# Kernel optimization log

Measured on AMD Instinct MI355X. Metric: run time of the kernel, lower is better.

The kernel has to match this reference:

```python
import jax, jax.numpy as jnp
import numpy as np

B, T1, T2, D = 16, 64, 64, 1024
PROJ = D // 2


def setup_inputs() -> dict:
    key = jax.random.key(0)
    k1, k2, k3 = jax.random.split(key, 3)
    x = jax.random.normal(k1, (B, T1, T2, D), dtype=jnp.float32)
    # glorot-style scale for params
    W_proj = jax.random.normal(k2, (D, PROJ), dtype=jnp.float32) * (2.0 / (D + PROJ)) ** 0.5
    v_score = jax.random.normal(k3, (PROJ,), dtype=jnp.float32) * (1.0 / PROJ) ** 0.5
    return {"x": x, "W_proj": W_proj, "v_score": v_score}


def reference(x, W_proj, v_score):
    # proj_input = tanh(tensordot(x, W_proj, axes=(3,0)))  -> (B, T1, T2, PROJ)
    proj = jnp.tanh(jnp.einsum('btsd,dp->btsp', x, W_proj))
    # att_scores = tensordot(proj, v_score, axes=(3,0))    -> (B, T1, T2)
    scores = jnp.einsum('btsp,p->bts', proj, v_score)
    # softmax over last axis (T2), weighted sum of x over T2 -> (B, T1, D)
    attn = jax.nn.softmax(scores, axis=-1)
    out = jnp.einsum('bts,btsd->btd', attn, x)
    return out
```

## Files before the change

### kernel.cpp

```cpp
#include <hip/hip_runtime.h>
#include <hip/hip_bf16.h>
#include <math.h>

#define B_    16
#define T1_   64
#define T2_   64
#define D_    1024
#define PROJ_ 512
#define BM    64
#define BK    32
#define NT    (D_ / BK)
#define LDP   40

typedef __attribute__((ext_vector_type(8))) short bf16x8;
typedef __attribute__((ext_vector_type(4))) float f32x4;
typedef __attribute__((ext_vector_type(4))) unsigned int u32x4;

__device__ __forceinline__ unsigned short f2bf(float f) {
  unsigned int u = __builtin_bit_cast(unsigned int, f);
  u += 0x7FFFu + ((u >> 16) & 1u);
  return (unsigned short)(u >> 16);
}

__device__ __forceinline__ float fast_tanh(float a) {
  float t = __builtin_amdgcn_exp2f(a * 2.885390081777927f);
  return 1.0f - 2.0f * __builtin_amdgcn_rcpf(t + 1.0f);
}

__global__ __launch_bounds__(256) void make_bfrag(
    const float* __restrict__ W, unsigned short* __restrict__ wt) {
  __shared__ float tile[32][33];
  const int t  = blockIdx.x;
  const int np = blockIdx.y;
  const int tx = threadIdx.x & 31;
  const int ty = threadIdx.x >> 5;
#pragma unroll
  for (int i = 0; i < 4; ++i)
    tile[ty + i * 8][tx] =
        W[(size_t)(t * 32 + ty + i * 8) * PROJ_ + np * 32 + tx];
  __syncthreads();
  if (threadIdx.x < 128) {
    const int sub  = threadIdx.x >> 6;
    const int lane = threadIdx.x & 63;
    const int llo = lane & 15, lhi = lane >> 4;
    unsigned short o[8];
#pragma unroll
    for (int j = 0; j < 8; ++j)
      o[j] = f2bf(tile[lhi * 8 + j][sub * 16 + llo]);
    const int n16 = np * 2 + sub;
    *(u32x4*)(wt + ((size_t)(t * 32 + n16) * 64 + lane) * 8) = *(const u32x4*)o;
  }
}

__global__ __launch_bounds__(512, 4) void fused_kernel(
    const float* __restrict__ x, const unsigned short* __restrict__ wt,
    const float* __restrict__ v, float* __restrict__ out) {
  __shared__ unsigned short As[2][BM][LDP];
  __shared__ float sp[BM][9];
  __shared__ float attn[BM];
  __shared__ f32x4 xred[256];

  const int tid  = threadIdx.x;
  const int lane = tid & 63;
  const int wid  = tid >> 6;
  const int llo  = lane & 15, lhi = lane >> 4;
  const int bt   = blockIdx.x;
  const int m0   = bt * BM;

  f32x4 acc[4][4];
#pragma unroll
  for (int mf = 0; mf < 4; ++mf)
#pragma unroll
    for (int nf = 0; nf < 4; ++nf) acc[mf][nf] = (f32x4){0.f, 0.f, 0.f, 0.f};

  const int arow = tid >> 3, akc = (tid & 7) * 4;
  const float* asrc = x + (size_t)(m0 + arow) * D_ + akc;

  const u32x4* wt4 = (const u32x4*)wt;
  const int bbase = (wid * 4) * 64 + lane;

  float4 s0 = *(const float4*)(asrc);
  float4 s1 = *(const float4*)(asrc + BK);
  u32x4 rb[4];
#pragma unroll
  for (int nf = 0; nf < 4; ++nf) rb[nf] = wt4[bbase + nf * 64];
  {
    ushort4 ua = {f2bf(s0.x), f2bf(s0.y), f2bf(s0.z), f2bf(s0.w)};
    *(ushort4*)&As[0][arow][akc] = ua;
  }

#define KSTEP(T, SLD, SCV, BR, BW)                                           \
  {                                                                          \
    __syncthreads();                                                         \
    bf16x8 af0 = *(const bf16x8*)&As[BR][ 0 + llo][lhi * 8];                 \
    bf16x8 af1 = *(const bf16x8*)&As[BR][16 + llo][lhi * 8];                 \
    bf16x8 af2 = *(const bf16x8*)&As[BR][32 + llo][lhi * 8];                 \
    bf16x8 af3 = *(const bf16x8*)&As[BR][48 + llo][lhi * 8];                 \
    if ((T) + 2 < NT) SLD = *(const float4*)(asrc + ((T) + 2) * BK);         \
    _Pragma("unroll")                                                        \
    for (int nf = 0; nf < 4; ++nf) {                                         \
      bf16x8 bfr = *(const bf16x8*)&rb[nf];                                  \
      acc[0][nf] = __builtin_amdgcn_mfma_f32_16x16x32_bf16(af0, bfr, acc[0][nf], 0, 0, 0); \
      acc[1][nf] = __builtin_amdgcn_mfma_f32_16x16x32_bf16(af1, bfr, acc[1][nf], 0, 0, 0); \
      acc[2][nf] = __builtin_amdgcn_mfma_f32_16x16x32_bf16(af2, bfr, acc[2][nf], 0, 0, 0); \
      acc[3][nf] = __builtin_amdgcn_mfma_f32_16x16x32_bf16(af3, bfr, acc[3][nf], 0, 0, 0); \
      if ((T) + 1 < NT) rb[nf] = wt4[bbase + ((T) + 1) * 2048 + nf * 64];    \
    }                                                                        \
    if ((T) + 1 < NT) {                                                      \
      ushort4 ua = {f2bf(SCV.x), f2bf(SCV.y), f2bf(SCV.z), f2bf(SCV.w)};     \
      *(ushort4*)&As[BW][arow][akc] = ua;                                    \
    }                                                                        \
  }

  for (int t = 0; t < NT; t += 2) {
    KSTEP(t,     s0, s1, 0, 1)
    KSTEP(t + 1, s1, s0, 1, 0)
  }
#undef KSTEP

  float vv0 = v[wid * 64 +  0 + llo];
  float vv1 = v[wid * 64 + 16 + llo];
  float vv2 = v[wid * 64 + 32 + llo];
  float vv3 = v[wid * 64 + 48 + llo];
#pragma unroll
  for (int mf = 0; mf < 4; ++mf) {
    float pr[4] = {0.f, 0.f, 0.f, 0.f};
#pragma unroll
    for (int r = 0; r < 4; ++r) {
      pr[r] += fast_tanh(acc[mf][0][r]) * vv0;
      pr[r] += fast_tanh(acc[mf][1][r]) * vv1;
      pr[r] += fast_tanh(acc[mf][2][r]) * vv2;
      pr[r] += fast_tanh(acc[mf][3][r]) * vv3;
    }
#pragma unroll
    for (int r = 0; r < 4; ++r) {
      float p = pr[r];
      p += __shfl_xor(p, 1, 64);
      p += __shfl_xor(p, 2, 64);
      p += __shfl_xor(p, 4, 64);
      p += __shfl_xor(p, 8, 64);
      if (llo == 0) sp[mf * 16 + lhi * 4 + r][wid] = p;
    }
  }
  __syncthreads();

  if (tid < BM) {
    float s = 0.f;
#pragma unroll
    for (int w = 0; w < 8; ++w) s += sp[tid][w];
    float mx = s;
#pragma unroll
    for (int mask = 1; mask < 64; mask <<= 1)
      mx = fmaxf(mx, __shfl_xor(mx, mask, 64));
    const float e = __builtin_amdgcn_exp2f((s - mx) * 1.442695040888963f);
    float sum = e;
#pragma unroll
    for (int mask = 1; mask < 64; mask <<= 1)
      sum += __shfl_xor(sum, mask, 64);
    attn[tid] = e * __builtin_amdgcn_rcpf(sum);
  }
  __syncthreads();

  const int c4 = tid & 255;
  const int sh = tid >> 8;
  const float* xg = x + ((size_t)m0 + sh * 32) * D_ + c4 * 4;
  f32x4 o0 = {0.f,0.f,0.f,0.f}, o1 = o0, o2 = o0, o3 = o0;
#pragma unroll
  for (int s = 0; s < 32; s += 4) {
    const float w0 = attn[sh * 32 + s + 0];
    const float w1 = attn[sh * 32 + s + 1];
    const float w2 = attn[sh * 32 + s + 2];
    const float w3 = attn[sh * 32 + s + 3];
    const float4 a0 = *(const float4*)(xg + (size_t)(s + 0) * D_);
    const float4 a1 = *(const float4*)(xg + (size_t)(s + 1) * D_);
    const float4 a2 = *(const float4*)(xg + (size_t)(s + 2) * D_);
    const float4 a3 = *(const float4*)(xg + (size_t)(s + 3) * D_);
    o0[0] += w0 * a0.x; o0[1] += w0 * a0.y; o0[2] += w0 * a0.z; o0[3] += w0 * a0.w;
    o1[0] += w1 * a1.x; o1[1] += w1 * a1.y; o1[2] += w1 * a1.z; o1[3] += w1 * a1.w;
    o2[0] += w2 * a2.x; o2[1] += w2 * a2.y; o2[2] += w2 * a2.z; o2[3] += w2 * a2.w;
    o3[0] += w3 * a3.x; o3[1] += w3 * a3.y; o3[2] += w3 * a3.z; o3[3] += w3 * a3.w;
  }
  f32x4 o;
#pragma unroll
  for (int j = 0; j < 4; ++j) o[j] = (o0[j] + o1[j]) + (o2[j] + o3[j]);
  if (sh == 1) xred[c4] = o;
  __syncthreads();
  if (sh == 0) {
    f32x4 o2b = xred[c4];
    float4 res = {o[0] + o2b[0], o[1] + o2b[1], o[2] + o2b[2], o[3] + o2b[3]};
    *(float4*)(out + (size_t)bt * D_ + c4 * 4) = res;
  }
}

extern "C" void kernel_launch(void* const* d_in, const int* in_sizes, int n_in,
                              void* d_out, int out_size, void* d_ws, size_t ws_size,
                              hipStream_t stream) {
  const float* x = (const float*)d_in[0];
  const float* W = (const float*)d_in[1];
  const float* v = (const float*)d_in[2];
  float* out = (float*)d_out;
  unsigned short* Wt = (unsigned short*)d_ws;

  make_bfrag<<<dim3(NT, PROJ_ / 32), 256, 0, stream>>>(W, Wt);
  fused_kernel<<<B_ * T1_, 512, 0, stream>>>(x, Wt, v, out);
}
```

Measured before the change: 113.9 us.

## Stage half of the K dimension into swizzled LDS in bulk instead of per-step double buffering

Replaces the per-32-K double-buffered A tile, which needed a barrier every step, with two bulk stages that each convert 512 columns of the 64-row x tile to bf16 into a 64KB XOR-swizzled LDS buffer. The MFMA loop then runs 16 steps per half with no barriers, prefetches the next W fragments, and raises wave priority around the MFMAs. This removes most of the barriers but loses overlap between global loads and compute inside each half, and the 64KB LDS allocation lowers occupancy below the launch-bounds target of 4 blocks.

Result: slower. 128.9 us (+13.2%).

```diff
diff --git a/kernel.cpp b/kernel.cpp
--- a/kernel.cpp
+++ b/kernel.cpp
@@ -8,9 +8,8 @@
 #define D_    1024
 #define PROJ_ 512
 #define BM    64
-#define BK    32
-#define NT    (D_ / BK)
-#define LDP   40
+#define NKH   16
+#define HALFK 512
 
 typedef __attribute__((ext_vector_type(8))) short bf16x8;
 typedef __attribute__((ext_vector_type(4))) float f32x4;
@@ -55,15 +54,16 @@
 __global__ __launch_bounds__(512, 4) void fused_kernel(
     const float* __restrict__ x, const unsigned short* __restrict__ wt,
     const float* __restrict__ v, float* __restrict__ out) {
-  __shared__ unsigned short As[2][BM][LDP];
-  __shared__ float sp[BM][9];
-  __shared__ float attn[BM];
-  __shared__ f32x4 xred[256];
+  __shared__ __align__(16) char smem[65536];
+  float (*sp)[9] = (float(*)[9])smem;
+  float* attn    = (float*)(smem + 2304);
+  f32x4* xred    = (f32x4*)(smem + 2560);
 
   const int tid  = threadIdx.x;
   const int lane = tid & 63;
   const int wid  = tid >> 6;
   const int llo  = lane & 15, lhi = lane >> 4;
+  const int swz  = (llo & 7) << 4;
   const int bt   = blockIdx.x;
   const int m0   = bt * BM;
 
@@ -73,73 +73,97 @@
 #pragma unroll
     for (int nf = 0; nf < 4; ++nf) acc[mf][nf] = (f32x4){0.f, 0.f, 0.f, 0.f};
 
-  const int arow = tid >> 3, akc = (tid & 7) * 4;
-  const float* asrc = x + (size_t)(m0 + arow) * D_ + akc;
-
   const u32x4* wt4 = (const u32x4*)wt;
   const int bbase = (wid * 4) * 64 + lane;
 
-  float4 s0 = *(const float4*)(asrc);
-  float4 s1 = *(const float4*)(asrc + BK);
   u32x4 rb[4];
 #pragma unroll
   for (int nf = 0; nf < 4; ++nf) rb[nf] = wt4[bbase + nf * 64];
+
+#define STAGE(H)                                                              \
+  {                                                                           \
+    _Pragma("unroll")                                                         \
+    for (int r = 0; r < 8; ++r) {                                             \
+      const int p = r * 512 + tid;                                            \
+      const int row = p >> 6, pc = p & 63;                                    \
+      const float* s = x + (size_t)(m0 + row) * D_ + (H) * HALFK + pc * 8;    \
+      float4 a = *(const float4*)s;                                           \
+      float4 b = *(const float4*)(s + 4);                                     \
+      unsigned short o[8] = {f2bf(a.x), f2bf(a.y), f2bf(a.z), f2bf(a.w),      \
+                             f2bf(b.x), f2bf(b.y), f2bf(b.z), f2bf(b.w)};     \
+      const int db = (row * 1024 + pc * 16) ^ ((row & 7) << 4);               \
+      *(u32x4*)(smem + db) = *(const u32x4*)o;                                \
+    }                                                                         \
+  }
+
+#define KLOOP(H)                                                              \
+  {                                                                           \
+    _Pragma("unroll 2")                                                       \
+    for (int ks = 0; ks < NKH; ++ks) {                                        \
+      const int t32 = (H) * NKH + ks;                                         \
+      const int kb = ks * 64 + lhi * 16;                                      \
+      bf16x8 af0 = *(const bf16x8*)(smem + ((( 0 + llo) * 1024 + kb) ^ swz)); \
+      bf16x8 af1 = *(const bf16x8*)(smem + (((16 + llo) * 1024 + kb) ^ swz)); \
+      bf16x8 af2 = *(const bf16x8*)(smem + (((32 + llo) * 1024 + kb) ^ swz)); \
+      bf16x8 af3 = *(const bf16x8*)(smem + (((48 + llo) * 1024 + kb) ^ swz)); \
+      u32x4 rbn[4];                                                           \
+      if (t32 + 1 < 32) {                                                     \
+        _Pragma("unroll")                                                     \
+        for (int nf = 0; nf < 4; ++nf)                                        \
+          rbn[nf] = wt4[(size_t)(t32 + 1) * 2048 + bbase + nf * 64];          \
+      }                                                                       \
+      __builtin_amdgcn_s_setprio(1);                                          \
+      _Pragma("unroll")                                                       \
+      for (int nf = 0; nf < 4; ++nf) {                                        \
+        bf16x8 bfr = *(const bf16x8*)&rb[nf];                                 \
+        acc[0][nf] = __builtin_amdgcn_mfma_f32_16x16x32_bf16(af0, bfr, acc[0][nf], 0, 0, 0); \
+        acc[1][nf] = __builtin_amdgcn_mfma_f32_16x16x32_bf16(af1, bfr, acc[1][nf], 0, 0, 0); \
+        acc[2][nf] = __builtin_amdgcn_mfma_f32_16x16x32_bf16(af2, bfr, acc[2][nf], 0, 0, 0); \
+        acc[3][nf] = __builtin_amdgcn_mfma_f32_16x16x32_bf16(af3, bfr, acc[3][nf], 0, 0, 0); \
+      }                                                                       \
+      __builtin_amdgcn_s_setprio(0);                                          \
+      if (t32 + 1 < 32) {                                                     \
+        _Pragma("unroll")                                                     \
+        for (int nf = 0; nf < 4; ++nf) rb[nf] = rbn[nf];                      \
+      }                                                                       \
+    }                                                                         \
+  }
+
+  STAGE(0)
+  __syncthreads();
+  KLOOP(0)
+  __syncthreads();
+  STAGE(1)
+  __syncthreads();
+  KLOOP(1)
+  __syncthreads();
+#undef STAGE
+#undef KLOOP
+
   {
-    ushort4 ua = {f2bf(s0.x), f2bf(s0.y), f2bf(s0.z), f2bf(s0.w)};
-    *(ushort4*)&As[0][arow][akc] = ua;
-  }
-
-#define KSTEP(T, SLD, SCV, BR, BW)                                           \
-  {                                                                          \
-    __syncthreads();                                                         \
-    bf16x8 af0 = *(const bf16x8*)&As[BR][ 0 + llo][lhi * 8];                 \
-    bf16x8 af1 = *(const bf16x8*)&As[BR][16 + llo][lhi * 8];                 \
-    bf16x8 af2 = *(const bf16x8*)&As[BR][32 + llo][lhi * 8];                 \
-    bf16x8 af3 = *(const bf16x8*)&As[BR][48 + llo][lhi * 8];                 \
-    if ((T) + 2 < NT) SLD = *(const float4*)(asrc + ((T) + 2) * BK);         \
-    _Pragma("unroll")                                                        \
-    for (int nf = 0; nf < 4; ++nf) {                                         \
-      bf16x8 bfr = *(const bf16x8*)&rb[nf];                                  \
-      acc[0][nf] = __builtin_amdgcn_mfma_f32_16x16x32_bf16(af0, bfr, acc[0][nf], 0, 0, 0); \
-      acc[1][nf] = __builtin_amdgcn_mfma_f32_16x16x32_bf16(af1, bfr, acc[1][nf], 0, 0, 0); \
-      acc[2][nf] = __builtin_amdgcn_mfma_f32_16x16x32_bf16(af2, bfr, acc[2][nf], 0, 0, 0); \
-      acc[3][nf] = __builtin_amdgcn_mfma_f32_16x16x32_bf16(af3, bfr, acc[3][nf], 0, 0, 0); \
-      if ((T) + 1 < NT) rb[nf] = wt4[bbase + ((T) + 1) * 2048 + nf * 64];    \
-    }                                                                        \
-    if ((T) + 1 < NT) {                                                      \
-      ushort4 ua = {f2bf(SCV.x), f2bf(SCV.y), f2bf(SCV.z), f2bf(SCV.w)};     \
-      *(ushort4*)&As[BW][arow][akc] = ua;                                    \
-    }                                                                        \
-  }
-
-  for (int t = 0; t < NT; t += 2) {
-    KSTEP(t,     s0, s1, 0, 1)
-    KSTEP(t + 1, s1, s0, 1, 0)
-  }
-#undef KSTEP
-
-  float vv0 = v[wid * 64 +  0 + llo];
-  float vv1 = v[wid * 64 + 16 + llo];
-  float vv2 = v[wid * 64 + 32 + llo];
-  float vv3 = v[wid * 64 + 48 + llo];
-#pragma unroll
-  for (int mf = 0; mf < 4; ++mf) {
-    float pr[4] = {0.f, 0.f, 0.f, 0.f};
-#pragma unroll
-    for (int r = 0; r < 4; ++r) {
-      pr[r] += fast_tanh(acc[mf][0][r]) * vv0;
-      pr[r] += fast_tanh(acc[mf][1][r]) * vv1;
-      pr[r] += fast_tanh(acc[mf][2][r]) * vv2;
-      pr[r] += fast_tanh(acc[mf][3][r]) * vv3;
-    }
-#pragma unroll
-    for (int r = 0; r < 4; ++r) {
-      float p = pr[r];
-      p += __shfl_xor(p, 1, 64);
-      p += __shfl_xor(p, 2, 64);
-      p += __shfl_xor(p, 4, 64);
-      p += __shfl_xor(p, 8, 64);
-      if (llo == 0) sp[mf * 16 + lhi * 4 + r][wid] = p;
+    const float vv0 = v[wid * 64 +  0 + llo];
+    const float vv1 = v[wid * 64 + 16 + llo];
+    const float vv2 = v[wid * 64 + 32 + llo];
+    const float vv3 = v[wid * 64 + 48 + llo];
+#pragma unroll
+    for (int mf = 0; mf < 4; ++mf) {
+      float pr[4] = {0.f, 0.f, 0.f, 0.f};
+#pragma unroll
+      for (int r = 0; r < 4; ++r) {
+        pr[r] += fast_tanh(acc[mf][0][r]) * vv0;
+        pr[r] += fast_tanh(acc[mf][1][r]) * vv1;
+        pr[r] += fast_tanh(acc[mf][2][r]) * vv2;
+        pr[r] += fast_tanh(acc[mf][3][r]) * vv3;
+      }
+#pragma unroll
+      for (int r = 0; r < 4; ++r) {
+        float p = pr[r];
+        p += __shfl_xor(p, 1, 64);
+        p += __shfl_xor(p, 2, 64);
+        p += __shfl_xor(p, 4, 64);
+        p += __shfl_xor(p, 8, 64);
+        if (llo == 0) sp[mf * 16 + lhi * 4 + r][wid] = p;
+      }
     }
   }
   __syncthreads();
@@ -201,6 +225,6 @@
   float* out = (float*)d_out;
   unsigned short* Wt = (unsigned short*)d_ws;
 
-  make_bfrag<<<dim3(NT, PROJ_ / 32), 256, 0, stream>>>(W, Wt);
+  make_bfrag<<<dim3(32, PROJ_ / 32), 256, 0, stream>>>(W, Wt);
   fused_kernel<<<B_ * T1_, 512, 0, stream>>>(x, Wt, v, out);
 }
```
